# Kernel tuning notes

Hardware: AMD Instinct MI355X
Metric: run time of the kernel (lower is better)

## Reference

```python
import jax, jax.numpy as jnp
import numpy as np

N, E, DIN, DOUT = 40000, 640000, 128, 10


def _gat_layer(h_in, src, dst, W, a_src, a_dst, b, n_nodes):
    # h: [N, D]; edges include self-loops already
    h = h_in @ W
    alpha = jax.nn.leaky_relu((h @ a_src)[src] + (h @ a_dst)[dst], 0.2)  # [E']
    m = jax.ops.segment_max(alpha, dst, num_segments=n_nodes)
    e = jnp.exp(alpha - m[dst])
    s = jax.ops.segment_sum(e, dst, num_segments=n_nodes)
    coef = e / (s[dst] + 1e-16)
    out = jax.ops.segment_sum(h[src] * coef[:, None], dst, num_segments=n_nodes)
    return out + b


def setup_inputs() -> dict:
    key = jax.random.key(0)
    ks = jax.random.split(key, 20)
    p = lambda k, shp: (jax.random.normal(k, shp, dtype=jnp.float32) * 0.05)
    inp = {
        "x": jax.random.normal(ks[0], (N, DIN), dtype=jnp.float32),
        "edge_index": jax.random.randint(ks[1], (2, E), 0, N, dtype=jnp.int32),
        "batch": jnp.sort(jax.random.randint(ks[2], (N,), 0, 64, dtype=jnp.int32)),
        "edge_attr": jax.random.normal(ks[3], (E, 4), dtype=jnp.float32),
        # GATConv 1: 128 -> 64
        "W1": p(ks[4], (DIN, 64)), "a1s": p(ks[5], (64,)), "a1d": p(ks[6], (64,)), "b1": jnp.zeros((64,), jnp.float32),
        # GATConv 2: 64 -> 128
        "W2": p(ks[7], (64, 128)), "a2s": p(ks[8], (128,)), "a2d": p(ks[9], (128,)), "b2": jnp.zeros((128,), jnp.float32),
        # GATConv 3: 128 -> 128
        "W3": p(ks[10], (128, 128)), "a3s": p(ks[11], (128,)), "a3d": p(ks[12], (128,)), "b3": jnp.zeros((128,), jnp.float32),
        # SAGPooling scorer: GraphConv(128, 1)
        "wp_rel": p(ks[13], (128, 1)), "wp_root": p(ks[14], (128, 1)), "bp": jnp.zeros((1,), jnp.float32),
        # final Linear(128, out_channels)
        "Wl": p(ks[15], (128, DOUT)), "bl": jnp.zeros((DOUT,), jnp.float32),
    }
    return inp


def reference(x, edge_index, batch, edge_attr,
              W1, a1s, a1d, b1, W2, a2s, a2d, b2, W3, a3s, a3d, b3,
              wp_rel, wp_root, bp, Wl, bl):
    n = x.shape[0]
    src, dst = edge_index[0], edge_index[1]
    # GATConv adds self-loops (edge_attr unused: edge_dim=None)
    loops = jnp.arange(n, dtype=src.dtype)
    src_sl = jnp.concatenate([src, loops])
    dst_sl = jnp.concatenate([dst, loops])

    h = jax.nn.relu(_gat_layer(x, src_sl, dst_sl, W1, a1s, a1d, b1, n))
    h = jax.nn.relu(_gat_layer(h, src_sl, dst_sl, W2, a2s, a2d, b2, n))
    h = jax.nn.relu(_gat_layer(h, src_sl, dst_sl, W3, a3s, a3d, b3, n))

    # SAGPooling(ratio=1): score via GraphConv (no self-loops), tanh gating, all nodes kept
    agg = jax.ops.segment_sum(h[src], dst, num_segments=n)  # [N, 128]
    score = (agg @ wp_rel + h @ wp_root + bp)[:, 0]         # [N]
    h = h * jnp.tanh(score)[:, None]

    # dropout is identity in eval mode
    return jax.nn.relu(h @ Wl + bl)
```

## Files before the change

### kernel.cpp

```cpp
#include <hip/hip_runtime.h>
#include <math.h>

template<int K, int N, int CPB>
__global__ __launch_bounds__(2 * CPB) void gemm_rt(
    const float* __restrict__ A, const float* __restrict__ B,
    float* __restrict__ C, int M,
    const float* __restrict__ iva, const float* __restrict__ ivb,
    float* __restrict__ ioa, float* __restrict__ iob)
{
    constexpr int KC = 32;
    constexpr int NC = K / KC;
    constexpr int TC = CPB / 8;
    constexpr int NT = 2 * CPB;
    constexpr int KT = KC / TC;
    constexpr int AST = 68;
    constexpr int A_F4 = 512 / NT;
    constexpr int B_F4 = (KC * CPB / 4) / NT;

    __shared__ float AsT[KC * AST];
    __shared__ float Bs[KC * CPB];

    const int tid = threadIdx.x;
    const int base = blockIdx.x * 64;
    const int col0 = blockIdx.y * CPB;
    const int tc = tid % TC;
    const int tr = tid / TC;

    float acc[4][8];
#pragma unroll
    for (int m = 0; m < 4; ++m)
#pragma unroll
        for (int j = 0; j < 8; ++j) acc[m][j] = 0.f;
    float sa[4], sb[4];
#pragma unroll
    for (int m = 0; m < 4; ++m) { sa[m] = 0.f; sb[m] = 0.f; }

    float4 ra[A_F4], rb[B_F4];

#pragma unroll
    for (int j = 0; j < A_F4; ++j) {
        int i = tid + j * NT; int row = i >> 3; int q = i & 7;
        int gr = base + row;
        ra[j] = (gr < M) ? *(const float4*)(A + (size_t)gr * K + 4 * q)
                         : make_float4(0.f, 0.f, 0.f, 0.f);
    }
#pragma unroll
    for (int j = 0; j < B_F4; ++j) {
        int i = tid + j * NT; int kk_ = i / (CPB / 4); int c4 = i % (CPB / 4);
        rb[j] = *(const float4*)(B + (size_t)kk_ * N + col0 + 4 * c4);
    }

    for (int ch = 0; ch < NC; ++ch) {
#pragma unroll
        for (int j = 0; j < A_F4; ++j) {
            int i = tid + j * NT; int row = i >> 3; int q = i & 7;
            AsT[(4 * q + 0) * AST + row] = ra[j].x;
            AsT[(4 * q + 1) * AST + row] = ra[j].y;
            AsT[(4 * q + 2) * AST + row] = ra[j].z;
            AsT[(4 * q + 3) * AST + row] = ra[j].w;
        }
#pragma unroll
        for (int j = 0; j < B_F4; ++j) {
            int i = tid + j * NT; int kk_ = i / (CPB / 4); int c4 = i % (CPB / 4);
            *(float4*)(Bs + kk_ * CPB + 4 * c4) = rb[j];
        }
        __syncthreads();

        if (ch + 1 < NC) {
            const int k0 = (ch + 1) * KC;
#pragma unroll
            for (int j = 0; j < A_F4; ++j) {
                int i = tid + j * NT; int row = i >> 3; int q = i & 7;
                int gr = base + row;
                ra[j] = (gr < M) ? *(const float4*)(A + (size_t)gr * K + k0 + 4 * q)
                                 : make_float4(0.f, 0.f, 0.f, 0.f);
            }
#pragma unroll
            for (int j = 0; j < B_F4; ++j) {
                int i = tid + j * NT; int kk_ = i / (CPB / 4); int c4 = i % (CPB / 4);
                rb[j] = *(const float4*)(B + (size_t)(k0 + kk_) * N + col0 + 4 * c4);
            }
        }

#pragma unroll 8
        for (int kk = 0; kk < KC; ++kk) {
            float4 a0 = *(const float4*)(AsT + kk * AST + 4 * tr);
            const float* bp = Bs + kk * CPB + 8 * tc;
            float4 b0 = *(const float4*)(bp);
            float4 b1 = *(const float4*)(bp + 4);
#pragma unroll
            for (int m = 0; m < 4; ++m) {
                float av = ((const float*)&a0)[m];
                acc[m][0] = fmaf(av, b0.x, acc[m][0]);
                acc[m][1] = fmaf(av, b0.y, acc[m][1]);
                acc[m][2] = fmaf(av, b0.z, acc[m][2]);
                acc[m][3] = fmaf(av, b0.w, acc[m][3]);
                acc[m][4] = fmaf(av, b1.x, acc[m][4]);
                acc[m][5] = fmaf(av, b1.y, acc[m][5]);
                acc[m][6] = fmaf(av, b1.z, acc[m][6]);
                acc[m][7] = fmaf(av, b1.w, acc[m][7]);
            }
        }

        if (iva != nullptr && blockIdx.y == 0) {
            const int k0 = ch * KC;
#pragma unroll
            for (int kl = 0; kl < KT; ++kl) {
                int k = tc * KT + kl;
                float av_ = iva[k0 + k];
                float bv_ = ivb[k0 + k];
#pragma unroll
                for (int m = 0; m < 4; ++m) {
                    float aval = AsT[k * AST + 4 * tr + m];
                    sa[m] = fmaf(aval, av_, sa[m]);
                    sb[m] = fmaf(aval, bv_, sb[m]);
                }
            }
        }
        __syncthreads();
    }

#pragma unroll
    for (int m = 0; m < 4; ++m) {
        int gr = base + 4 * tr + m;
        if (gr < M) {
            *(float4*)(C + (size_t)gr * N + col0 + 8 * tc) =
                make_float4(acc[m][0], acc[m][1], acc[m][2], acc[m][3]);
            *(float4*)(C + (size_t)gr * N + col0 + 8 * tc + 4) =
                make_float4(acc[m][4], acc[m][5], acc[m][6], acc[m][7]);
        }
    }
    if (iva != nullptr && blockIdx.y == 0) {
#pragma unroll
        for (int m = 0; m < 4; ++m) {
#pragma unroll
            for (int off = TC / 2; off; off >>= 1) {
                sa[m] += __shfl_xor(sa[m], off);
                sb[m] += __shfl_xor(sb[m], off);
            }
        }
        if (tc == 0) {
#pragma unroll
            for (int m = 0; m < 4; ++m) {
                int gr = base + 4 * tr + m;
                if (gr < M) { ioa[gr] = sa[m]; iob[gr] = sb[m]; }
            }
        }
    }
}

template<int K, int N, int NT>
__global__ __launch_bounds__(256) void gemm_tile(
    const float* __restrict__ A, const float* __restrict__ B,
    float* __restrict__ C, int M,
    const float* __restrict__ bias, const float* __restrict__ score, int outN)
{
    __shared__ float As[64 * K];
    const int tid = threadIdx.x;
    const int base = blockIdx.x * 64;
    for (int idx = tid; idx < 64 * K; idx += 256) {
        int r = idx / K, k = idx - r * K;
        int gr = base + r;
        As[idx] = (gr < M) ? A[(size_t)gr * K + k] : 0.f;
    }
    __syncthreads();
    constexpr int RSTEP = 256 / NT;
    constexpr int NR = 64 / RSTEP;
    const int c = tid % NT;
    const int r0 = tid / NT;
    float acc[NR];
#pragma unroll
    for (int i = 0; i < NR; ++i) acc[i] = 0.f;
    const float4* As4 = reinterpret_cast<const float4*>(As);
    const float* Bc = B + c;
    float b0 = Bc[0 * N], b1 = Bc[1 * N], b2 = Bc[2 * N], b3 = Bc[3 * N];
    for (int k = 0; k < K; k += 4) {
        const int kn = (k + 4 < K) ? (k + 4) : k;
        float n0 = Bc[(kn + 0) * N];
        float n1 = Bc[(kn + 1) * N];
        float n2 = Bc[(kn + 2) * N];
        float n3 = Bc[(kn + 3) * N];
#pragma unroll
        for (int i = 0; i < NR; ++i) {
            float4 a = As4[((r0 + i * RSTEP) * K + k) >> 2];
            acc[i] = fmaf(a.x, b0, acc[i]);
            acc[i] = fmaf(a.y, b1, acc[i]);
            acc[i] = fmaf(a.z, b2, acc[i]);
            acc[i] = fmaf(a.w, b3, acc[i]);
        }
        b0 = n0; b1 = n1; b2 = n2; b3 = n3;
    }
    if (c < outN) {
#pragma unroll
        for (int i = 0; i < NR; ++i) {
            int gr = base + r0 + i * RSTEP;
            if (gr < M) {
                float v = tanhf(score[gr]) * acc[i] + bias[c];
                C[(size_t)gr * outN + c] = fmaxf(v, 0.f);
            }
        }
    }
}

__global__ __launch_bounds__(256) void hist_deg(
    const int* __restrict__ dst, int* __restrict__ deg, int E)
{
    int e = blockIdx.x * 256 + threadIdx.x;
    if (e < E) atomicAdd(deg + dst[e], 1);
}

__global__ __launch_bounds__(256) void scan_local(
    const int* __restrict__ deg, int* __restrict__ row_start, int* __restrict__ blocksum, int n)
{
    __shared__ int s[256];
    const int t = threadIdx.x;
    const int i = blockIdx.x * 256 + t;
    int v = (i < n) ? deg[i] : 0;
    s[t] = v;
    __syncthreads();
#pragma unroll
    for (int off = 1; off < 256; off <<= 1) {
        int u = (t >= off) ? s[t - off] : 0;
        __syncthreads();
        s[t] += u;
        __syncthreads();
    }
    if (i < n) row_start[i] = s[t] - v;
    if (t == 255) blocksum[blockIdx.x] = s[255];
}

__global__ __launch_bounds__(256) void scan_blocks(int* __restrict__ blocksum, int nb)
{
    __shared__ int s[256];
    const int t = threadIdx.x;
    int v = (t < nb) ? blocksum[t] : 0;
    s[t] = v;
    __syncthreads();
#pragma unroll
    for (int off = 1; off < 256; off <<= 1) {
        int u = (t >= off) ? s[t - off] : 0;
        __syncthreads();
        s[t] += u;
        __syncthreads();
    }
    if (t < nb) blocksum[t] = s[t] - v;
}

__global__ __launch_bounds__(256) void scan_add(
    int* __restrict__ row_start, int* __restrict__ cursor,
    const int* __restrict__ blocksum, int n, int total)
{
    const int i = blockIdx.x * 256 + threadIdx.x;
    if (i < n) {
        int v = row_start[i] + blocksum[blockIdx.x];
        row_start[i] = v;
        cursor[i] = v;
    } else if (i == n) {
        row_start[n] = total;
    }
}

__global__ __launch_bounds__(256) void fill_csr(
    const int* __restrict__ src, const int* __restrict__ dst,
    int* __restrict__ cursor, int* __restrict__ csr_src, int E)
{
    int e = blockIdx.x * 256 + threadIdx.x;
    if (e >= E) return;
    int pos = atomicAdd(cursor + dst[e], 1);
    csr_src[pos] = src[e];
}

template<int D, bool POOL>
__global__ __launch_bounds__(256) void gat_aggregate(
    const int* __restrict__ row_start, const int* __restrict__ csr_src,
    const float* __restrict__ asv, const float* __restrict__ adv,
    const float* __restrict__ h, const float* __restrict__ bias,
    float* __restrict__ out,
    const float* __restrict__ wpr, const float* __restrict__ wpo,
    float* __restrict__ poolA, float* __restrict__ poolB, int n)
{
    __shared__ float lds_e[4][128];
    __shared__ int   lds_i[4][128];
    const int node = (blockIdx.x * 256 + threadIdx.x) >> 6;
    const int lane = threadIdx.x & 63;
    const int w = threadIdx.x >> 6;
    if (node >= n) return;
    const int beg = row_start[node];
    const int deg = row_start[node + 1] - beg;
    const float advv = adv[node];
    const bool fast = (deg <= 128);

    float a_self = asv[node] + advv;
    a_self = (a_self >= 0.f) ? a_self : 0.2f * a_self;
    const float ev_self = expf(a_self);

    float ssum = (lane == 0) ? ev_self : 0.f;
    if (fast) {
        for (int j = lane; j < deg; j += 64) {
            int s = csr_src[beg + j];
            lds_i[w][j] = s;
            float a = asv[s] + advv;
            a = (a >= 0.f) ? a : 0.2f * a;
            float ev = expf(a);
            lds_e[w][j] = ev;
            ssum += ev;
        }
    } else {
        for (int j = lane; j < deg; j += 64) {
            float a = asv[csr_src[beg + j]] + advv;
            a = (a >= 0.f) ? a : 0.2f * a;
            ssum += expf(a);
        }
    }
#pragma unroll
    for (int off = 32; off; off >>= 1) ssum += __shfl_xor(ssum, off);
    const float inv = 1.f / (ssum + 1e-16f);

    if (fast) {
        if constexpr (D == 128) {
            const float4* h4 = reinterpret_cast<const float4*>(h);
            const int half = lane >> 5;
            const int fl = lane & 31;
            float4 a0 = {0,0,0,0}, a1 = {0,0,0,0}, a2 = {0,0,0,0}, a3 = {0,0,0,0};
            int j = 0;
            for (; j + 8 <= deg; j += 8) {
                int e0 = j + half, e1 = j + 2 + half, e2 = j + 4 + half, e3 = j + 6 + half;
                int s0 = lds_i[w][e0], s1 = lds_i[w][e1], s2 = lds_i[w][e2], s3 = lds_i[w][e3];
                float c0 = lds_e[w][e0] * inv, c1 = lds_e[w][e1] * inv;
                float c2 = lds_e[w][e2] * inv, c3 = lds_e[w][e3] * inv;
                float4 v0 = h4[(size_t)s0 * 32 + fl];
                float4 v1 = h4[(size_t)s1 * 32 + fl];
                float4 v2 = h4[(size_t)s2 * 32 + fl];
                float4 v3 = h4[(size_t)s3 * 32 + fl];
                a0.x = fmaf(v0.x, c0, a0.x); a0.y = fmaf(v0.y, c0, a0.y);
                a0.z = fmaf(v0.z, c0, a0.z); a0.w = fmaf(v0.w, c0, a0.w);
                a1.x = fmaf(v1.x, c1, a1.x); a1.y = fmaf(v1.y, c1, a1.y);
                a1.z = fmaf(v1.z, c1, a1.z); a1.w = fmaf(v1.w, c1, a1.w);
                a2.x = fmaf(v2.x, c2, a2.x); a2.y = fmaf(v2.y, c2, a2.y);
                a2.z = fmaf(v2.z, c2, a2.z); a2.w = fmaf(v2.w, c2, a2.w);
                a3.x = fmaf(v3.x, c3, a3.x); a3.y = fmaf(v3.y, c3, a3.y);
                a3.z = fmaf(v3.z, c3, a3.z); a3.w = fmaf(v3.w, c3, a3.w);
            }
            for (; j < deg; j += 2) {
                int e = j + half;
                bool ok = (e < deg);
                int s = lds_i[w][ok ? e : 0];
                float c = ok ? lds_e[w][e] * inv : 0.f;
                float4 v = h4[(size_t)s * 32 + fl];
                a0.x = fmaf(v.x, c, a0.x); a0.y = fmaf(v.y, c, a0.y);
                a0.z = fmaf(v.z, c, a0.z); a0.w = fmaf(v.w, c, a0.w);
            }
            {
                float c = (half == 0) ? ev_self * inv : 0.f;
                float4 v = h4[(size_t)node * 32 + fl];
                a1.x = fmaf(v.x, c, a1.x); a1.y = fmaf(v.y, c, a1.y);
                a1.z = fmaf(v.z, c, a1.z); a1.w = fmaf(v.w, c, a1.w);
            }
            float4 t;
            t.x = (a0.x + a1.x) + (a2.x + a3.x);
            t.y = (a0.y + a1.y) + (a2.y + a3.y);
            t.z = (a0.z + a1.z) + (a2.z + a3.z);
            t.w = (a0.w + a1.w) + (a2.w + a3.w);
            t.x += __shfl_xor(t.x, 32);
            t.y += __shfl_xor(t.y, 32);
            t.z += __shfl_xor(t.z, 32);
            t.w += __shfl_xor(t.w, 32);
            const float4 b4 = reinterpret_cast<const float4*>(bias)[fl];
            float4 o;
            o.x = fmaxf(t.x + b4.x, 0.f);
            o.y = fmaxf(t.y + b4.y, 0.f);
            o.z = fmaxf(t.z + b4.z, 0.f);
            o.w = fmaxf(t.w + b4.w, 0.f);
            if (half == 0)
                reinterpret_cast<float4*>(out)[(size_t)node * 32 + fl] = o;
            if constexpr (POOL) {
                const float4 r4 = reinterpret_cast<const float4*>(wpr)[fl];
                const float4 q4 = reinterpret_cast<const float4*>(wpo)[fl];
                float pa = o.x * r4.x + o.y * r4.y + o.z * r4.z + o.w * r4.w;
                float pb = o.x * q4.x + o.y * q4.y + o.z * q4.z + o.w * q4.w;
#pragma unroll
                for (int off = 16; off; off >>= 1) {
                    pa += __shfl_xor(pa, off);
                    pb += __shfl_xor(pb, off);
                }
                if (lane == 0) { poolA[node] = pa; poolB[node] = pb; }
            }
        } else {
            const float4* h4 = reinterpret_cast<const float4*>(h);
            const int q = lane >> 4;
            const int fl = lane & 15;
            float4 a0 = {0,0,0,0}, a1 = {0,0,0,0};
            int j = 0;
            for (; j + 8 <= deg; j += 8) {
                int e0 = j + q, e1 = j + 4 + q;
                int s0 = lds_i[w][e0], s1 = lds_i[w][e1];
                float c0 = lds_e[w][e0] * inv, c1 = lds_e[w][e1] * inv;
                float4 v0 = h4[(size_t)s0 * 16 + fl];
                float4 v1 = h4[(size_t)s1 * 16 + fl];
                a0.x = fmaf(v0.x, c0, a0.x); a0.y = fmaf(v0.y, c0, a0.y);
                a0.z = fmaf(v0.z, c0, a0.z); a0.w = fmaf(v0.w, c0, a0.w);
                a1.x = fmaf(v1.x, c1, a1.x); a1.y = fmaf(v1.y, c1, a1.y);
                a1.z = fmaf(v1.z, c1, a1.z); a1.w = fmaf(v1.w, c1, a1.w);
            }
            for (; j < deg; j += 4) {
                int e = j + q;
                bool ok = (e < deg);
                int s = lds_i[w][ok ? e : 0];
                float c = ok ? lds_e[w][e] * inv : 0.f;
                float4 v = h4[(size_t)s * 16 + fl];
                a0.x = fmaf(v.x, c, a0.x); a0.y = fmaf(v.y, c, a0.y);
                a0.z = fmaf(v.z, c, a0.z); a0.w = fmaf(v.w, c, a0.w);
            }
            {
                float c = (q == 0) ? ev_self * inv : 0.f;
                float4 v = h4[(size_t)node * 16 + fl];
                a1.x = fmaf(v.x, c, a1.x); a1.y = fmaf(v.y, c, a1.y);
                a1.z = fmaf(v.z, c, a1.z); a1.w = fmaf(v.w, c, a1.w);
            }
            float4 t;
            t.x = a0.x + a1.x; t.y = a0.y + a1.y; t.z = a0.z + a1.z; t.w = a0.w + a1.w;
            t.x += __shfl_xor(t.x, 16); t.x += __shfl_xor(t.x, 32);
            t.y += __shfl_xor(t.y, 16); t.y += __shfl_xor(t.y, 32);
            t.z += __shfl_xor(t.z, 16); t.z += __shfl_xor(t.z, 32);
            t.w += __shfl_xor(t.w, 16); t.w += __shfl_xor(t.w, 32);
            const float4 b4 = reinterpret_cast<const float4*>(bias)[fl];
            float4 o;
            o.x = fmaxf(t.x + b4.x, 0.f);
            o.y = fmaxf(t.y + b4.y, 0.f);
            o.z = fmaxf(t.z + b4.z, 0.f);
            o.w = fmaxf(t.w + b4.w, 0.f);
            if (q == 0)
                reinterpret_cast<float4*>(out)[(size_t)node * 16 + fl] = o;
        }
    } else {
        if constexpr (D == 128) {
            const float2* h2 = reinterpret_cast<const float2*>(h);
            float2 a0 = {0.f, 0.f};
            for (int j = 0; j < deg; ++j) {
                int s = csr_src[beg + j];
                float a = asv[s] + advv;
                a = (a >= 0.f) ? a : 0.2f * a;
                float c = expf(a) * inv;
                float2 v = h2[(size_t)s * 64 + lane];
                a0.x = fmaf(v.x, c, a0.x); a0.y = fmaf(v.y, c, a0.y);
            }
            {
                float c = ev_self * inv;
                float2 v = h2[(size_t)node * 64 + lane];
                a0.x = fmaf(v.x, c, a0.x); a0.y = fmaf(v.y, c, a0.y);
            }
            float2 o;
            o.x = fmaxf(a0.x + bias[2 * lane], 0.f);
            o.y = fmaxf(a0.y + bias[2 * lane + 1], 0.f);
            reinterpret_cast<float2*>(out)[(size_t)node * 64 + lane] = o;
            if constexpr (POOL) {
                float pa = fmaf(o.x, wpr[2 * lane], o.y * wpr[2 * lane + 1]);
                float pb = fmaf(o.x, wpo[2 * lane], o.y * wpo[2 * lane + 1]);
#pragma unroll
                for (int off = 32; off; off >>= 1) {
                    pa += __shfl_xor(pa, off);
                    pb += __shfl_xor(pb, off);
                }
                if (lane == 0) { poolA[node] = pa; poolB[node] = pb; }
            }
        } else {
            float a0 = 0.f;
            for (int j = 0; j < deg; ++j) {
                int s = csr_src[beg + j];
                float a = asv[s] + advv;
                a = (a >= 0.f) ? a : 0.2f * a;
                a0 = fmaf(h[(size_t)s * D + lane], expf(a) * inv, a0);
            }
            a0 = fmaf(h[(size_t)node * D + lane], ev_self * inv, a0);
            out[(size_t)node * D + lane] = fmaxf(a0 + bias[lane], 0.f);
        }
    }
}

__global__ __launch_bounds__(256) void score_csr(
    const int* __restrict__ row_start, const int* __restrict__ csr_src,
    const float* __restrict__ ts, const float* __restrict__ td,
    const float* __restrict__ bp, float* __restrict__ score, int n)
{
    int i = blockIdx.x * 256 + threadIdx.x;
    if (i >= n) return;
    int beg = row_start[i], end = row_start[i + 1];
    float s = td[i] + bp[0];
    for (int j = beg; j < end; ++j) s += ts[csr_src[j]];
    score[i] = s;
}

__global__ __launch_bounds__(256) void precompute(
    const float* __restrict__ W1, const float* __restrict__ a1s, const float* __restrict__ a1d,
    const float* __restrict__ W2, const float* __restrict__ a2s, const float* __restrict__ a2d,
    const float* __restrict__ W3, const float* __restrict__ a3s, const float* __restrict__ a3d,
    const float* __restrict__ Wl, const float* __restrict__ bl,
    float* __restrict__ va1, float* __restrict__ vb1,
    float* __restrict__ va2, float* __restrict__ vb2,
    float* __restrict__ va3, float* __restrict__ vb3,
    float* __restrict__ Wlp, float* __restrict__ blp,
    int* __restrict__ deg, int n)
{
    int t = blockIdx.x * 256 + threadIdx.x;
    if (t < n) deg[t] = 0;
    if (t < 128) {
        float sa = 0.f, sb = 0.f;
        for (int j = 0; j < 64; ++j) {
            float w = W1[t * 64 + j];
            sa = fmaf(w, a1s[j], sa); sb = fmaf(w, a1d[j], sb);
        }
        va1[t] = sa; vb1[t] = sb;
    } else if (t < 192) {
        int k = t - 128;
        float sa = 0.f, sb = 0.f;
        for (int j = 0; j < 128; ++j) {
            float w = W2[k * 128 + j];
            sa = fmaf(w, a2s[j], sa); sb = fmaf(w, a2d[j], sb);
        }
        va2[k] = sa; vb2[k] = sb;
    } else if (t < 320) {
        int k = t - 192;
        float sa = 0.f, sb = 0.f;
        for (int j = 0; j < 128; ++j) {
            float w = W3[k * 128 + j];
            sa = fmaf(w, a3s[j], sa); sb = fmaf(w, a3d[j], sb);
        }
        va3[k] = sa; vb3[k] = sb;
    } else if (t < 320 + 2048) {
        int i = t - 320;
        int k = i >> 4, c = i & 15;
        Wlp[i] = (c < 10) ? Wl[k * 10 + c] : 0.f;
    } else if (t < 320 + 2048 + 16) {
        int c = t - (320 + 2048);
        blp[c] = (c < 10) ? bl[c] : 0.f;
    }
}

extern "C" void kernel_launch(void* const* d_in, const int* in_sizes, int n_in,
                              void* d_out, int out_size, void* d_ws, size_t ws_size,
                              hipStream_t stream) {
    const float* x   = (const float*)d_in[0];
    const int*   ei  = (const int*)d_in[1];
    const float* W1  = (const float*)d_in[4];
    const float* a1s = (const float*)d_in[5];
    const float* a1d = (const float*)d_in[6];
    const float* b1  = (const float*)d_in[7];
    const float* W2  = (const float*)d_in[8];
    const float* a2s = (const float*)d_in[9];
    const float* a2d = (const float*)d_in[10];
    const float* b2  = (const float*)d_in[11];
    const float* W3  = (const float*)d_in[12];
    const float* a3s = (const float*)d_in[13];
    const float* a3d = (const float*)d_in[14];
    const float* b3  = (const float*)d_in[15];
    const float* wpr = (const float*)d_in[16];
    const float* wpo = (const float*)d_in[17];
    const float* bp  = (const float*)d_in[18];
    const float* Wl  = (const float*)d_in[19];
    const float* bl  = (const float*)d_in[20];

    const int n = in_sizes[0] / 128;
    const int E = in_sizes[1] / 2;
    const int* src = ei;
    const int* dst = ei + E;

    float* ws = (float*)d_ws;
    const size_t nd = (size_t)n * 128;
    float* bufA      = ws;
    float* bufB      = bufA + nd;
    float* asv       = bufB + nd;
    float* adv       = asv + n;
    float* tsv       = adv + n;
    float* tdv       = tsv + n;
    float* score     = tdv + n;
    int*   deg       = (int*)(score + n);
    int*   row_start = deg + n;
    int*   cursor    = row_start + n + 1;
    int*   blocksum  = cursor + n;
    int*   csr_src   = blocksum + 256;
    float* va1       = (float*)(csr_src + E);
    float* vb1       = va1 + 128;
    float* va2       = vb1 + 128;
    float* vb2       = va2 + 64;
    float* va3       = vb2 + 64;
    float* vb3       = va3 + 128;
    float* Wlp       = vb3 + 128;
    float* blp       = Wlp + 128 * 16;

    const unsigned EB = (unsigned)((E + 255) / 256);
    const unsigned NB = (unsigned)((n + 255) / 256);
    const unsigned MB = (unsigned)((n + 63) / 64);
    const unsigned WB = (unsigned)(((size_t)n * 64 + 255) / 256);

    precompute<<<NB, 256, 0, stream>>>(W1, a1s, a1d, W2, a2s, a2d, W3, a3s, a3d, Wl, bl,
                                       va1, vb1, va2, vb2, va3, vb3, Wlp, blp, deg, n);
    hist_deg<<<EB, 256, 0, stream>>>(dst, deg, E);
    scan_local<<<NB, 256, 0, stream>>>(deg, row_start, blocksum, n);
    scan_blocks<<<1, 256, 0, stream>>>(blocksum, (int)NB);
    scan_add<<<NB, 256, 0, stream>>>(row_start, cursor, blocksum, n, E);
    fill_csr<<<EB, 256, 0, stream>>>(src, dst, cursor, csr_src, E);

    gemm_rt<128, 64, 64><<<dim3(MB, 1), 128, 0, stream>>>(
        x, W1, bufA, n, va1, vb1, asv, adv);
    gat_aggregate<64, false><<<WB, 256, 0, stream>>>(row_start, csr_src, asv, adv, bufA, b1, bufB,
                                                     nullptr, nullptr, nullptr, nullptr, n);

    gemm_rt<64, 128, 64><<<dim3(MB, 2), 128, 0, stream>>>(
        bufB, W2, bufA, n, va2, vb2, asv, adv);
    gat_aggregate<128, false><<<WB, 256, 0, stream>>>(row_start, csr_src, asv, adv, bufA, b2, bufB,
                                                      nullptr, nullptr, nullptr, nullptr, n);

    gemm_rt<128, 128, 64><<<dim3(MB, 2), 128, 0, stream>>>(
        bufB, W3, bufA, n, va3, vb3, asv, adv);
    gat_aggregate<128, true><<<WB, 256, 0, stream>>>(row_start, csr_src, asv, adv, bufA, b3, bufB,
                                                     wpr, wpo, tsv, tdv, n);

    score_csr<<<NB, 256, 0, stream>>>(row_start, csr_src, tsv, tdv, bp, score, n);
    gemm_tile<128, 16, 16><<<MB, 256, 0, stream>>>(bufB, Wlp, (float*)d_out, n, blp, score, 10);
}
```

Baseline: 296.3 us.

## Split GAT aggregation into coefficient pass and column-sliced SpMM kernel

```diff
diff --git a/kernel.cpp b/kernel.cpp
--- a/kernel.cpp
+++ b/kernel.cpp
@@ -202,6 +202,29 @@
     }
 }
 
+template<int D>
+__global__ __launch_bounds__(256) void node_dots(
+    const float* __restrict__ h, const float* __restrict__ va, const float* __restrict__ vb,
+    float* __restrict__ outa, float* __restrict__ outb, int n)
+{
+    int node = (blockIdx.x * 256 + threadIdx.x) >> 6;
+    int lane = threadIdx.x & 63;
+    if (node >= n) return;
+    float sa = 0.f, sb = 0.f;
+#pragma unroll
+    for (int f = lane; f < D; f += 64) {
+        float hv = h[(size_t)node * D + f];
+        sa = fmaf(hv, va[f], sa);
+        sb = fmaf(hv, vb[f], sb);
+    }
+#pragma unroll
+    for (int off = 32; off; off >>= 1) {
+        sa += __shfl_xor(sa, off);
+        sb += __shfl_xor(sb, off);
+    }
+    if (lane == 0) { outa[node] = sa; outb[node] = sb; }
+}
+
 __global__ __launch_bounds__(256) void hist_deg(
     const int* __restrict__ dst, int* __restrict__ deg, int E)
 {
@@ -270,210 +293,87 @@
     csr_src[pos] = src[e];
 }
 
-template<int D, bool POOL>
-__global__ __launch_bounds__(256) void gat_aggregate(
+__global__ __launch_bounds__(256) void gat_coef(
     const int* __restrict__ row_start, const int* __restrict__ csr_src,
     const float* __restrict__ asv, const float* __restrict__ adv,
-    const float* __restrict__ h, const float* __restrict__ bias,
-    float* __restrict__ out,
-    const float* __restrict__ wpr, const float* __restrict__ wpo,
-    float* __restrict__ poolA, float* __restrict__ poolB, int n)
-{
-    __shared__ float lds_e[4][128];
-    __shared__ int   lds_i[4][128];
+    float* __restrict__ coef, float* __restrict__ selfc, int n)
+{
     const int node = (blockIdx.x * 256 + threadIdx.x) >> 6;
     const int lane = threadIdx.x & 63;
-    const int w = threadIdx.x >> 6;
     if (node >= n) return;
     const int beg = row_start[node];
     const int deg = row_start[node + 1] - beg;
     const float advv = adv[node];
-    const bool fast = (deg <= 128);
-
     float a_self = asv[node] + advv;
     a_self = (a_self >= 0.f) ? a_self : 0.2f * a_self;
     const float ev_self = expf(a_self);
-
     float ssum = (lane == 0) ? ev_self : 0.f;
-    if (fast) {
-        for (int j = lane; j < deg; j += 64) {
-            int s = csr_src[beg + j];
-            lds_i[w][j] = s;
-            float a = asv[s] + advv;
-            a = (a >= 0.f) ? a : 0.2f * a;
-            float ev = expf(a);
-            lds_e[w][j] = ev;
-            ssum += ev;
-        }
-    } else {
-        for (int j = lane; j < deg; j += 64) {
-            float a = asv[csr_src[beg + j]] + advv;
-            a = (a >= 0.f) ? a : 0.2f * a;
-            ssum += expf(a);
-        }
+    for (int j = lane; j < deg; j += 64) {
+        float a = asv[csr_src[beg + j]] + advv;
+        a = (a >= 0.f) ? a : 0.2f * a;
+        float ev = expf(a);
+        coef[beg + j] = ev;
+        ssum += ev;
     }
 #pragma unroll
     for (int off = 32; off; off >>= 1) ssum += __shfl_xor(ssum, off);
     const float inv = 1.f / (ssum + 1e-16f);
-
-    if (fast) {
-        if constexpr (D == 128) {
-            const float4* h4 = reinterpret_cast<const float4*>(h);
-            const int half = lane >> 5;
-            const int fl = lane & 31;
-            float4 a0 = {0,0,0,0}, a1 = {0,0,0,0}, a2 = {0,0,0,0}, a3 = {0,0,0,0};
-            int j = 0;
-            for (; j + 8 <= deg; j += 8) {
-                int e0 = j + half, e1 = j + 2 + half, e2 = j + 4 + half, e3 = j + 6 + half;
-                int s0 = lds_i[w][e0], s1 = lds_i[w][e1], s2 = lds_i[w][e2], s3 = lds_i[w][e3];
-                float c0 = lds_e[w][e0] * inv, c1 = lds_e[w][e1] * inv;
-                float c2 = lds_e[w][e2] * inv, c3 = lds_e[w][e3] * inv;
-                float4 v0 = h4[(size_t)s0 * 32 + fl];
-                float4 v1 = h4[(size_t)s1 * 32 + fl];
-                float4 v2 = h4[(size_t)s2 * 32 + fl];
-                float4 v3 = h4[(size_t)s3 * 32 + fl];
-                a0.x = fmaf(v0.x, c0, a0.x); a0.y = fmaf(v0.y, c0, a0.y);
-                a0.z = fmaf(v0.z, c0, a0.z); a0.w = fmaf(v0.w, c0, a0.w);
-                a1.x = fmaf(v1.x, c1, a1.x); a1.y = fmaf(v1.y, c1, a1.y);
-                a1.z = fmaf(v1.z, c1, a1.z); a1.w = fmaf(v1.w, c1, a1.w);
-                a2.x = fmaf(v2.x, c2, a2.x); a2.y = fmaf(v2.y, c2, a2.y);
-                a2.z = fmaf(v2.z, c2, a2.z); a2.w = fmaf(v2.w, c2, a2.w);
-                a3.x = fmaf(v3.x, c3, a3.x); a3.y = fmaf(v3.y, c3, a3.y);
-                a3.z = fmaf(v3.z, c3, a3.z); a3.w = fmaf(v3.w, c3, a3.w);
-            }
-            for (; j < deg; j += 2) {
-                int e = j + half;
-                bool ok = (e < deg);
-                int s = lds_i[w][ok ? e : 0];
-                float c = ok ? lds_e[w][e] * inv : 0.f;
-                float4 v = h4[(size_t)s * 32 + fl];
-                a0.x = fmaf(v.x, c, a0.x); a0.y = fmaf(v.y, c, a0.y);
-                a0.z = fmaf(v.z, c, a0.z); a0.w = fmaf(v.w, c, a0.w);
-            }
-            {
-                float c = (half == 0) ? ev_self * inv : 0.f;
-                float4 v = h4[(size_t)node * 32 + fl];
-                a1.x = fmaf(v.x, c, a1.x); a1.y = fmaf(v.y, c, a1.y);
-                a1.z = fmaf(v.z, c, a1.z); a1.w = fmaf(v.w, c, a1.w);
-            }
-            float4 t;
-            t.x = (a0.x + a1.x) + (a2.x + a3.x);
-            t.y = (a0.y + a1.y) + (a2.y + a3.y);
-            t.z = (a0.z + a1.z) + (a2.z + a3.z);
-            t.w = (a0.w + a1.w) + (a2.w + a3.w);
-            t.x += __shfl_xor(t.x, 32);
-            t.y += __shfl_xor(t.y, 32);
-            t.z += __shfl_xor(t.z, 32);
-            t.w += __shfl_xor(t.w, 32);
-            const float4 b4 = reinterpret_cast<const float4*>(bias)[fl];
-            float4 o;
-            o.x = fmaxf(t.x + b4.x, 0.f);
-            o.y = fmaxf(t.y + b4.y, 0.f);
-            o.z = fmaxf(t.z + b4.z, 0.f);
-            o.w = fmaxf(t.w + b4.w, 0.f);
-            if (half == 0)
-                reinterpret_cast<float4*>(out)[(size_t)node * 32 + fl] = o;
-            if constexpr (POOL) {
-                const float4 r4 = reinterpret_cast<const float4*>(wpr)[fl];
-                const float4 q4 = reinterpret_cast<const float4*>(wpo)[fl];
-                float pa = o.x * r4.x + o.y * r4.y + o.z * r4.z + o.w * r4.w;
-                float pb = o.x * q4.x + o.y * q4.y + o.z * q4.z + o.w * q4.w;
-#pragma unroll
-                for (int off = 16; off; off >>= 1) {
-                    pa += __shfl_xor(pa, off);
-                    pb += __shfl_xor(pb, off);
-                }
-                if (lane == 0) { poolA[node] = pa; poolB[node] = pb; }
-            }
-        } else {
-            const float4* h4 = reinterpret_cast<const float4*>(h);
-            const int q = lane >> 4;
-            const int fl = lane & 15;
-            float4 a0 = {0,0,0,0}, a1 = {0,0,0,0};
-            int j = 0;
-            for (; j + 8 <= deg; j += 8) {
-                int e0 = j + q, e1 = j + 4 + q;
-                int s0 = lds_i[w][e0], s1 = lds_i[w][e1];
-                float c0 = lds_e[w][e0] * inv, c1 = lds_e[w][e1] * inv;
-                float4 v0 = h4[(size_t)s0 * 16 + fl];
-                float4 v1 = h4[(size_t)s1 * 16 + fl];
-                a0.x = fmaf(v0.x, c0, a0.x); a0.y = fmaf(v0.y, c0, a0.y);
-                a0.z = fmaf(v0.z, c0, a0.z); a0.w = fmaf(v0.w, c0, a0.w);
-                a1.x = fmaf(v1.x, c1, a1.x); a1.y = fmaf(v1.y, c1, a1.y);
-                a1.z = fmaf(v1.z, c1, a1.z); a1.w = fmaf(v1.w, c1, a1.w);
-            }
-            for (; j < deg; j += 4) {
-                int e = j + q;
-                bool ok = (e < deg);
-                int s = lds_i[w][ok ? e : 0];
-                float c = ok ? lds_e[w][e] * inv : 0.f;
-                float4 v = h4[(size_t)s * 16 + fl];
-                a0.x = fmaf(v.x, c, a0.x); a0.y = fmaf(v.y, c, a0.y);
-                a0.z = fmaf(v.z, c, a0.z); a0.w = fmaf(v.w, c, a0.w);
-            }
-            {
-                float c = (q == 0) ? ev_self * inv : 0.f;
-                float4 v = h4[(size_t)node * 16 + fl];
-                a1.x = fmaf(v.x, c, a1.x); a1.y = fmaf(v.y, c, a1.y);
-                a1.z = fmaf(v.z, c, a1.z); a1.w = fmaf(v.w, c, a1.w);
-            }
-            float4 t;
-            t.x = a0.x + a1.x; t.y = a0.y + a1.y; t.z = a0.z + a1.z; t.w = a0.w + a1.w;
-            t.x += __shfl_xor(t.x, 16); t.x += __shfl_xor(t.x, 32);
-            t.y += __shfl_xor(t.y, 16); t.y += __shfl_xor(t.y, 32);
-            t.z += __shfl_xor(t.z, 16); t.z += __shfl_xor(t.z, 32);
-            t.w += __shfl_xor(t.w, 16); t.w += __shfl_xor(t.w, 32);
-            const float4 b4 = reinterpret_cast<const float4*>(bias)[fl];
-            float4 o;
-            o.x = fmaxf(t.x + b4.x, 0.f);
-            o.y = fmaxf(t.y + b4.y, 0.f);
-            o.z = fmaxf(t.z + b4.z, 0.f);
-            o.w = fmaxf(t.w + b4.w, 0.f);
-            if (q == 0)
-                reinterpret_cast<float4*>(out)[(size_t)node * 16 + fl] = o;
-        }
-    } else {
-        if constexpr (D == 128) {
-            const float2* h2 = reinterpret_cast<const float2*>(h);
-            float2 a0 = {0.f, 0.f};
-            for (int j = 0; j < deg; ++j) {
-                int s = csr_src[beg + j];
-                float a = asv[s] + advv;
-                a = (a >= 0.f) ? a : 0.2f * a;
-                float c = expf(a) * inv;
-                float2 v = h2[(size_t)s * 64 + lane];
-                a0.x = fmaf(v.x, c, a0.x); a0.y = fmaf(v.y, c, a0.y);
-            }
-            {
-                float c = ev_self * inv;
-                float2 v = h2[(size_t)node * 64 + lane];
-                a0.x = fmaf(v.x, c, a0.x); a0.y = fmaf(v.y, c, a0.y);
-            }
-            float2 o;
-            o.x = fmaxf(a0.x + bias[2 * lane], 0.f);
-            o.y = fmaxf(a0.y + bias[2 * lane + 1], 0.f);
-            reinterpret_cast<float2*>(out)[(size_t)node * 64 + lane] = o;
-            if constexpr (POOL) {
-                float pa = fmaf(o.x, wpr[2 * lane], o.y * wpr[2 * lane + 1]);
-                float pb = fmaf(o.x, wpo[2 * lane], o.y * wpo[2 * lane + 1]);
-#pragma unroll
-                for (int off = 32; off; off >>= 1) {
-                    pa += __shfl_xor(pa, off);
-                    pb += __shfl_xor(pb, off);
-                }
-                if (lane == 0) { poolA[node] = pa; poolB[node] = pb; }
-            }
-        } else {
-            float a0 = 0.f;
-            for (int j = 0; j < deg; ++j) {
-                int s = csr_src[beg + j];
-                float a = asv[s] + advv;
-                a = (a >= 0.f) ? a : 0.2f * a;
-                a0 = fmaf(h[(size_t)s * D + lane], expf(a) * inv, a0);
-            }
-            a0 = fmaf(h[(size_t)node * D + lane], ev_self * inv, a0);
-            out[(size_t)node * D + lane] = fmaxf(a0 + bias[lane], 0.f);
-        }
+    for (int j = lane; j < deg; j += 64) coef[beg + j] *= inv;
+    if (lane == 0) selfc[node] = ev_self * inv;
+}
+
+template<int D, int NSLICE>
+__global__ __launch_bounds__(256) void gat_spmm(
+    const int* __restrict__ row_start, const int* __restrict__ csr_src,
+    const float* __restrict__ coef, const float* __restrict__ selfc,
+    const float* __restrict__ h, const float* __restrict__ bias,
+    float* __restrict__ out, int n)
+{
+    const int slice = blockIdx.x % NSLICE;
+    const int ngrp = blockIdx.x / NSLICE;
+    const int node = ngrp * 4 + (threadIdx.x >> 6);
+    const int lane = threadIdx.x & 63;
+    if (node >= n) return;
+    const int g = lane >> 2;
+    const int sub = lane & 3;
+    const int beg = row_start[node];
+    const int deg = row_start[node + 1] - beg;
+    const float4* h4 = reinterpret_cast<const float4*>(h);
+    const int scol = slice * 4 + sub;
+
+    float4 acc = {0.f, 0.f, 0.f, 0.f};
+    for (int j = g; j < deg; j += 16) {
+        int s = csr_src[beg + j];
+        float c = coef[beg + j];
+        float4 v = h4[(size_t)s * (D / 4) + scol];
+        acc.x = fmaf(v.x, c, acc.x);
+        acc.y = fmaf(v.y, c, acc.y);
+        acc.z = fmaf(v.z, c, acc.z);
+        acc.w = fmaf(v.w, c, acc.w);
+    }
+    if (g == 0) {
+        float c = selfc[node];
+        float4 v = h4[(size_t)node * (D / 4) + scol];
+        acc.x = fmaf(v.x, c, acc.x);
+        acc.y = fmaf(v.y, c, acc.y);
+        acc.z = fmaf(v.z, c, acc.z);
+        acc.w = fmaf(v.w, c, acc.w);
+    }
+#pragma unroll
+    for (int off = 4; off <= 32; off <<= 1) {
+        acc.x += __shfl_xor(acc.x, off);
+        acc.y += __shfl_xor(acc.y, off);
+        acc.z += __shfl_xor(acc.z, off);
+        acc.w += __shfl_xor(acc.w, off);
+    }
+    if (g == 0) {
+        float4 b = reinterpret_cast<const float4*>(bias)[scol];
+        float4 o;
+        o.x = fmaxf(acc.x + b.x, 0.f);
+        o.y = fmaxf(acc.y + b.y, 0.f);
+        o.z = fmaxf(acc.z + b.z, 0.f);
+        o.w = fmaxf(acc.w + b.w, 0.f);
+        reinterpret_cast<float4*>(out)[(size_t)node * (D / 4) + scol] = o;
     }
 }
 
@@ -573,12 +473,14 @@
     float* tsv       = adv + n;
     float* tdv       = tsv + n;
     float* score     = tdv + n;
-    int*   deg       = (int*)(score + n);
+    float* selfc     = score + n;
+    int*   deg       = (int*)(selfc + n);
     int*   row_start = deg + n;
     int*   cursor    = row_start + n + 1;
     int*   blocksum  = cursor + n;
     int*   csr_src   = blocksum + 256;
-    float* va1       = (float*)(csr_src + E);
+    float* coef      = (float*)(csr_src + E);
+    float* va1       = coef + E;
     float* vb1       = va1 + 128;
     float* va2       = vb1 + 128;
     float* vb2       = va2 + 64;
@@ -591,6 +493,7 @@
     const unsigned NB = (unsigned)((n + 255) / 256);
     const unsigned MB = (unsigned)((n + 63) / 64);
     const unsigned WB = (unsigned)(((size_t)n * 64 + 255) / 256);
+    const unsigned GB = (unsigned)((n + 3) / 4);
 
     precompute<<<NB, 256, 0, stream>>>(W1, a1s, a1d, W2, a2s, a2d, W3, a3s, a3d, Wl, bl,
                                        va1, vb1, va2, vb2, va3, vb3, Wlp, blp, deg, n);
@@ -602,19 +505,23 @@
 
     gemm_rt<128, 64, 64><<<dim3(MB, 1), 128, 0, stream>>>(
         x, W1, bufA, n, va1, vb1, asv, adv);
-    gat_aggregate<64, false><<<WB, 256, 0, stream>>>(row_start, csr_src, asv, adv, bufA, b1, bufB,
-                                                     nullptr, nullptr, nullptr, nullptr, n);
+    gat_coef<<<WB, 256, 0, stream>>>(row_start, csr_src, asv, adv, coef, selfc, n);
+    gat_spmm<64, 4><<<GB * 4, 256, 0, stream>>>(row_start, csr_src, coef, selfc,
+                                                bufA, b1, bufB, n);
 
     gemm_rt<64, 128, 64><<<dim3(MB, 2), 128, 0, stream>>>(
         bufB, W2, bufA, n, va2, vb2, asv, adv);
-    gat_aggregate<128, false><<<WB, 256, 0, stream>>>(row_start, csr_src, asv, adv, bufA, b2, bufB,
-                                                      nullptr, nullptr, nullptr, nullptr, n);
+    gat_coef<<<WB, 256, 0, stream>>>(row_start, csr_src, asv, adv, coef, selfc, n);
+    gat_spmm<128, 8><<<GB * 8, 256, 0, stream>>>(row_start, csr_src, coef, selfc,
+                                                 bufA, b2, bufB, n);
 
     gemm_rt<128, 128, 64><<<dim3(MB, 2), 128, 0, stream>>>(
         bufB, W3, bufA, n, va3, vb3, asv, adv);
-    gat_aggregate<128, true><<<WB, 256, 0, stream>>>(row_start, csr_src, asv, adv, bufA, b3, bufB,
-                                                     wpr, wpo, tsv, tdv, n);
-
+    gat_coef<<<WB, 256, 0, stream>>>(row_start, csr_src, asv, adv, coef, selfc, n);
+    gat_spmm<128, 8><<<GB * 8, 256, 0, stream>>>(row_start, csr_src, coef, selfc,
+                                                 bufA, b3, bufB, n);
+
+    node_dots<128><<<WB, 256, 0, stream>>>(bufB, wpr, wpo, tsv, tdv, n);
     score_csr<<<NB, 256, 0, stream>>>(row_start, csr_src, tsv, tdv, bp, score, n);
     gemm_tile<128, 16, 16><<<MB, 256, 0, stream>>>(bufB, Wlp, (float*)d_out, n, blp, score, 10);
 }
```

Measured after the change: 492.4 us. 1.66x slower.
